# Optimization experiments

Measured on AMD Instinct MI355X. Metric: run time of the kernel, lower is better.

## Reference

```python
import jax, jax.numpy as jnp
import numpy as np

BS, L, D = 16, 256, 512
H, DQ, DV, DFF, KSZ = 8, 64, 64, 2048, 3


def _ln(x, g, b, eps=1e-5):
    mu = jnp.mean(x, -1, keepdims=True)
    var = jnp.mean((x - mu) ** 2, -1, keepdims=True)
    return (x - mu) / jnp.sqrt(var + eps) * g + b


def _conv(x, w):
    # x: [bs, 1, d] (NCW), w: [1, 1, k], same padding for odd k, no bias
    pad = (w.shape[-1] - 1) // 2
    return jax.lax.conv_general_dilated(x, w, (1,), [(pad, pad)], dimension_numbers=('NCH', 'OIH', 'NCH'))


def setup_inputs() -> dict:
    key = jax.random.key(0)
    ks = jax.random.split(key, 12)
    s = lambda k, shape, sc: jax.random.normal(k, shape, jnp.float32) * sc
    w0 = 0.02
    return {
        'inp': jax.random.normal(ks[0], (BS, L, D), jnp.float32),
        'conv1_w': s(ks[1], (1, 1, KSZ), 0.3),
        'conv2_w': s(ks[2], (1, 1, KSZ), 0.3),
        'ctx_wq': s(ks[3], (D, H * DQ), w0),
        'ctx_wk': s(ks[4], (D, H * DQ), w0),
        'ctx_fc': s(ks[5], (H * DV, D), w0),
        'glb_wq': s(ks[6], (D, H * DQ), w0),
        'glb_wk': s(ks[7], (D, H * DQ), w0),
        'glb_fc': s(ks[8], (H * DV, D), w0),
        'ln1_g': jnp.ones(D), 'ln1_b': jnp.zeros(D),
        'ln2_g': jnp.ones(D), 'ln2_b': jnp.zeros(D),
        'ln3_g': jnp.ones(D), 'ln3_b': jnp.zeros(D),
        'mlp_w1': s(ks[9], (D, DFF), w0), 'mlp_b1': jnp.zeros(DFF),
        'mlp_w2': s(ks[10], (DFF, D), w0), 'mlp_b2': jnp.zeros(D),
    }


def reference(inp, conv1_w, conv2_w, ctx_wq, ctx_wk, ctx_fc,
              glb_wq, glb_wk, glb_fc, ln1_g, ln1_b, ln2_g, ln2_b,
              ln3_g, ln3_b, mlp_w1, mlp_b1, mlp_w2, mlp_b2):
    bs, seqlen, d = inp.shape
    scale = 1.0 / jnp.sqrt(jnp.float32(DQ))
    # Global K/V are step-invariant: hoist out of the recurrence.
    # NOTE: original module (faithfully) projects V with W_Q, not W_V.
    Kg = (inp @ glb_wk).reshape(bs, seqlen, H, DQ).transpose(0, 2, 1, 3)  # [b,h,L,dq]
    Vg = (inp @ glb_wq).reshape(bs, seqlen, H, DV).transpose(0, 2, 1, 3)  # [b,h,L,dv]

    def step(hn, x_i):
        # hn: [bs,1,d] recurrent state, x_i: [bs,d] current token
        x = x_i[:, None, :]                                   # [bs,1,d]
        res = x
        xc = _conv(x, conv1_w)                                # [bs,1,d]
        # context cross-attn: Q=hn, K=xc, V=xc (via W_Q, as in source)
        Qc = (hn @ ctx_wq).reshape(bs, 1, H, DQ).transpose(0, 2, 1, 3)
        Kc = (xc @ ctx_wk).reshape(bs, 1, H, DQ).transpose(0, 2, 1, 3)
        Vc = (xc @ ctx_wq).reshape(bs, 1, H, DV).transpose(0, 2, 1, 3)
        sc = jnp.einsum('bhqd,bhkd->bhqk', Qc, Kc) * scale    # [b,h,1,1]
        ac = jax.nn.softmax(sc, axis=-1)
        ctx = jnp.einsum('bhqk,bhkd->bhqd', ac, Vc)
        ctx = ctx.transpose(0, 2, 1, 3).reshape(bs, 1, H * DV) @ ctx_fc
        x = _ln(ctx + res, ln1_g, ln1_b)
        res = x
        x2 = _conv(x, conv2_w)
        # global cross-attn: Q=x2, K/V from full input (hoisted)
        Qg = (x2 @ glb_wq).reshape(bs, 1, H, DQ).transpose(0, 2, 1, 3)
        sg = jnp.einsum('bhqd,bhkd->bhqk', Qg, Kg) * scale    # [b,h,1,L]
        h = jnp.einsum('bhqk,bhkd->bhqd', jax.nn.softmax(sg, axis=-1), Vg)
        h = h.transpose(0, 2, 1, 3).reshape(bs, 1, H * DV) @ glb_fc  # [bs,1,d]
        x = _ln(h + res, ln2_g, ln2_b)
        y = jax.nn.gelu(x @ mlp_w1 + mlp_b1, approximate=False) @ mlp_w2 + mlp_b2
        y = _ln(y + x, ln3_g, ln3_b)
        return h, y[:, 0, :]

    hn0 = inp[:, 0:1, :]
    hn, ys = jax.lax.scan(step, hn0, jnp.swapaxes(inp, 0, 1))  # ys: [L,bs,d]
    output = jnp.swapaxes(ys, 0, 1)                            # [bs,L,d]
    return output, hn
```

## Files before the change

### kernel.cpp

```cpp
#include <hip/hip_runtime.h>
#include <math.h>

#define NBS 16
#define NL 256
#define ND 512
#define NH 8
#define NDFF 2048
#define NT (NBS*NL)

typedef unsigned short u16;
typedef unsigned int   u32;
typedef __attribute__((ext_vector_type(8))) short bf16x8;
typedef __attribute__((ext_vector_type(4))) float f32x4;

__device__ __forceinline__ u16 f2b(float f){
  u32 u = __float_as_uint(f);
  u32 r = u + 0x7FFFu + ((u >> 16) & 1u);
  return (u16)(r >> 16);
}
__device__ __forceinline__ float blo(u32 u){ return __uint_as_float(u << 16); }
__device__ __forceinline__ float bhi(u32 u){ return __uint_as_float(u & 0xFFFF0000u); }
__device__ __forceinline__ float b2f(u16 v){ return __uint_as_float(((u32)v) << 16); }
__device__ __forceinline__ u32 pk2(float a, float b){ return (u32)f2b(a) | ((u32)f2b(b) << 16); }

__device__ __forceinline__ void gl16(const void* g, void* l){
  __builtin_amdgcn_global_load_lds((const __attribute__((address_space(1))) void*)g,
                                   (__attribute__((address_space(3))) void*)l, 16, 0, 0);
}
__device__ __forceinline__ float gelu_f(float x){ return 0.5f*x*(1.f+erff(x*0.70710678118654752f)); }

__device__ inline void tr_tile(const float* __restrict__ src, u16* __restrict__ dst,
                               int K, int N, int ntk, int tb, float* Tsh){
  int tk = tb % ntk, tn = tb / ntk;
  int t = threadIdx.x;
  int r = t >> 2, q = t & 3;
  const float* s = src + (size_t)(tk*64 + r)*N + tn*64 + q*16;
  #pragma unroll
  for (int u2 = 0; u2 < 4; u2++){
    float4 v = *(const float4*)(s + u2*4);
    Tsh[r*65 + q*16 + u2*4 + 0] = v.x;
    Tsh[r*65 + q*16 + u2*4 + 1] = v.y;
    Tsh[r*65 + q*16 + u2*4 + 2] = v.z;
    Tsh[r*65 + q*16 + u2*4 + 3] = v.w;
  }
  __syncthreads();
  int n = t >> 2, kq = t & 3;
  u16* d = dst + (size_t)(tn*64 + n)*K + tk*64 + kq*16;
  u32 u[8];
  #pragma unroll
  for (int j = 0; j < 8; j++){
    u32 lo = f2b(Tsh[(kq*16 + 2*j    )*65 + n]);
    u32 hi = f2b(Tsh[(kq*16 + 2*j + 1)*65 + n]);
    u[j] = lo | (hi << 16);
  }
  ((uint4*)d)[0] = make_uint4(u[0],u[1],u[2],u[3]);
  ((uint4*)d)[1] = make_uint4(u[4],u[5],u[6],u[7]);
}

__global__ __launch_bounds__(256) void pack_k(
    const float* __restrict__ inp,
    const float* __restrict__ ctx_wq, const float* __restrict__ ctx_fc,
    const float* __restrict__ glb_wq, const float* __restrict__ glb_wk,
    const float* __restrict__ glb_fc,
    const float* __restrict__ w1, const float* __restrict__ w2,
    const float* __restrict__ c1w,
    u16* wk_t, u16* wq_t, u16* cfc_t, u16* gfc_t, u16* cwq_bf,
    u16* w1_t, u16* w2_t, u16* inp_bf, u16* xc_bf)
{
  __shared__ float Tsh[64*65];
  int bx = blockIdx.x, t = threadIdx.x;
  if (bx < 256){
    int m = bx >> 6, tb = bx & 63;
    const float* s; u16* d;
    if      (m == 0){ s = glb_wk; d = wk_t; }
    else if (m == 1){ s = glb_wq; d = wq_t; }
    else if (m == 2){ s = ctx_fc; d = cfc_t; }
    else            { s = glb_fc; d = gfc_t; }
    tr_tile(s, d, 512, 512, 8, tb, Tsh);
  } else if (bx < 512){
    tr_tile(w1, w1_t, 512, 2048, 8, bx - 256, Tsh);
  } else if (bx < 768){
    tr_tile(w2, w2_t, 2048, 512, 32, bx - 512, Tsh);
  } else if (bx < 1792){
    size_t i0 = (size_t)(bx - 768)*2048 + (size_t)t*8;
    float4 v0 = *(const float4*)(inp + i0);
    float4 v1 = *(const float4*)(inp + i0 + 4);
    uint4 o;
    o.x = pk2(v0.x, v0.y); o.y = pk2(v0.z, v0.w);
    o.z = pk2(v1.x, v1.y); o.w = pk2(v1.z, v1.w);
    *(uint4*)(inp_bf + i0) = o;
  } else if (bx < 2816){
    size_t i0 = (size_t)(bx - 1792)*2048 + (size_t)t*8;
    float w0 = c1w[0], w1v = c1w[1], w2v = c1w[2];
    u32 u[4];
    #pragma unroll
    for (int j = 0; j < 8; j += 2){
      float f[2];
      #pragma unroll
      for (int s2 = 0; s2 < 2; s2++){
        size_t i = i0 + j + s2; int d = (int)(i & (ND-1));
        float xm = d        ? inp[i-1] : 0.f;
        float x0 = inp[i];
        float xp = (d<ND-1) ? inp[i+1] : 0.f;
        f[s2] = w0*xm + w1v*x0 + w2v*xp;
      }
      u[j>>1] = pk2(f[0], f[1]);
    }
    *(uint4*)(xc_bf + i0) = make_uint4(u[0],u[1],u[2],u[3]);
  } else {
    size_t i0 = (size_t)(bx - 2816)*2048 + (size_t)t*8;
    float4 v0 = *(const float4*)(ctx_wq + i0);
    float4 v1 = *(const float4*)(ctx_wq + i0 + 4);
    uint4 o;
    o.x = pk2(v0.x, v0.y); o.y = pk2(v0.z, v0.w);
    o.z = pk2(v1.x, v1.y); o.w = pk2(v1.z, v1.w);
    *(uint4*)(cwq_bf + i0) = o;
  }
}

template<int TM,int BIAS,int ACT>
__device__ __forceinline__ void gemm_core(const u16* __restrict__ A,
    const u16* __restrict__ Bt, const float* __restrict__ bias,
    void* __restrict__ Cb, int N, int K, int lda, int ldb, int outm,
    u16* sm, int row0, int col0)
{
  constexpr int MF = TM/32;
  constexpr int ABUF = TM*128;
  constexpr int NLD = TM/32 + 2;
  const int tid = threadIdx.x;
  const int w = tid >> 6, l = tid & 63;
  const int wr = w >> 1, wc = w & 1;
  const int srow = tid >> 3;
  const int scol = (((tid & 7)*16) ^ ((srow & 7) << 4)) >> 1;
  const u16* pa = A  + (size_t)(row0 + srow)*lda + scol;
  const u16* pb = Bt + (size_t)(col0 + srow)*ldb + scol;
  char* lA0 = (char*)sm + (tid & ~63)*16;
  char* lB0 = (char*)sm + 3*ABUF + (tid & ~63)*16;

  f32x4 acc[MF][2] = {};
  const int l15 = l & 15, lk = (l >> 4)*16;
  const int nt = K >> 6;

  auto STAGE = [&](int buf, int kt){
    char* lA = lA0 + buf*ABUF;
    char* lB = lB0 + buf*8192;
    #pragma unroll
    for (int i = 0; i < TM/32; i++)
      gl16(pa + kt*64 + (size_t)(i*32)*lda, lA + i*4096);
    gl16(pb + kt*64,                  lB);
    gl16(pb + kt*64 + (size_t)32*ldb, lB + 4096);
  };

  STAGE(0, 0);
  int cur = 0, nxt = 1;
  for (int t = 0; t < nt; ++t){
    if (t + 1 < nt){
      STAGE(nxt, t + 1);
      if constexpr (NLD == 4) asm volatile("s_waitcnt vmcnt(4)" ::: "memory");
      else                    asm volatile("s_waitcnt vmcnt(6)" ::: "memory");
    } else {
      asm volatile("s_waitcnt vmcnt(0)" ::: "memory");
    }
    __builtin_amdgcn_s_barrier();
    __builtin_amdgcn_sched_barrier(0);
    const char* bA = (const char*)sm + cur*ABUF;
    const char* bB = (const char*)sm + 3*ABUF + cur*8192;
    #pragma unroll
    for (int ks = 0; ks < 2; ks++){
      bf16x8 af[MF], bv[2];
      #pragma unroll
      for (int m = 0; m < MF; m++){
        int r = wr*(TM/2) + m*16 + l15;
        int cb = (ks*64 + lk) ^ ((r & 7) << 4);
        af[m] = *(const bf16x8*)(bA + r*128 + cb);
      }
      #pragma unroll
      for (int n = 0; n < 2; n++){
        int r = wc*32 + n*16 + l15;
        int cb = (ks*64 + lk) ^ ((r & 7) << 4);
        bv[n] = *(const bf16x8*)(bB + r*128 + cb);
      }
      #pragma unroll
      for (int m = 0; m < MF; m++)
        #pragma unroll
        for (int n = 0; n < 2; n++)
          acc[m][n] = __builtin_amdgcn_mfma_f32_16x16x32_bf16(af[m], bv[n], acc[m][n], 0, 0, 0);
    }
    cur = nxt; nxt = (nxt == 2) ? 0 : nxt + 1;
  }

  #pragma unroll
  for (int m = 0; m < MF; m++){
    #pragma unroll
    for (int n = 0; n < 2; n++){
      int col = col0 + wc*32 + n*16 + l15;
      int rowb = row0 + wr*(TM/2) + m*16 + (l >> 4)*4;
      if (outm == 2){
        uint2 o;
        o.x = pk2(acc[m][n][0], acc[m][n][1]);
        o.y = pk2(acc[m][n][2], acc[m][n][3]);
        *(uint2*)((u16*)Cb + (size_t)(rowb >> 8)*131072 + (size_t)col*256 + (rowb & 255)) = o;
      } else if (outm == 0){
        #pragma unroll
        for (int rr = 0; rr < 4; rr++)
          ((float*)Cb)[(size_t)(rowb + rr)*N + col] = acc[m][n][rr];
      } else {
        #pragma unroll
        for (int rr = 0; rr < 4; rr++){
          float v = acc[m][n][rr];
          if (BIAS) v += bias[col];
          if (ACT)  v = gelu_f(v);
          ((u16*)Cb)[(size_t)(rowb + rr)*N + col] = f2b(v);
        }
      }
    }
  }
}

template<int TM,int BIAS,int ACT,int OUTM>
__global__ __launch_bounds__(256) void gemm_k(const u16* __restrict__ A,
                                              const u16* __restrict__ Bt,
                                              const float* __restrict__ bias,
                                              void* __restrict__ Cb,
                                              int N, int K)
{
  __shared__ u16 sm[3*(TM*128 + 8192)/2];
  gemm_core<TM,BIAS,ACT>(A, Bt, bias, Cb, N, K, K, K, OUTM, sm,
                         blockIdx.y*TM, blockIdx.x*64);
}

__global__ __launch_bounds__(256) void gemm3_k(
    const u16* __restrict__ A0, const u16* __restrict__ B0, u16* __restrict__ C0,
    const u16* __restrict__ A1, const u16* __restrict__ B1, u16* __restrict__ C1,
    const u16* __restrict__ A2, const u16* __restrict__ B2, u16* __restrict__ C2)
{
  __shared__ u16 sm[3*(64*128 + 8192)/2];
  const u16 *A, *Bt; u16* Cb; int outm = 1;
  if (blockIdx.z == 0){ A = A0; Bt = B0; Cb = C0; }
  else if (blockIdx.z == 1){ A = A1; Bt = B1; Cb = C1; outm = 2; }
  else { A = A2; Bt = B2; Cb = C2; }
  gemm_core<64,0,0>(A, Bt, nullptr, Cb, 512, 512, 512, 512, outm, sm,
                    blockIdx.y*64, blockIdx.x*64);
}

__global__ __launch_bounds__(256) void gemm_w2sk(const u16* __restrict__ G,
                                                 const u16* __restrict__ w2t,
                                                 float* __restrict__ P)
{
  __shared__ u16 sm[3*(128*128 + 8192)/2];
  const int z = blockIdx.z;
  gemm_core<128,0,0>(G + z*1024, w2t + z*1024, nullptr,
                     (void*)(P + (size_t)z*NT*512), 512, 1024, 2048, 2048, 0,
                     sm, blockIdx.y*128, blockIdx.x*64);
}

__global__ __launch_bounds__(256) void attn_k(const u16* __restrict__ Q,
                                              const u16* __restrict__ Kg,
                                              const u16* __restrict__ Vt,
                                              u16* __restrict__ O){
  __shared__ u16 sm[36864];
  const int bh = blockIdx.x, b = bh >> 3, h = bh & 7;
  const int tid = threadIdx.x;
  const int w = tid >> 6, l = tid & 63;
  const int l15 = l & 15, lg = l >> 4;
  const int qt0 = b*NL + blockIdx.y*64 + w*16;

  {
    const int srow = tid >> 3;
    const int scolK = (((tid & 7)*16) ^ ((srow & 7) << 4)) >> 1;
    const u16* pk = Kg + (size_t)(b*NL + srow)*ND + h*64 + scolK;
    char* lK = (char*)sm + (tid & ~63)*16;
    #pragma unroll
    for (int c = 0; c < 8; c++)
      gl16(pk + (size_t)(c*32)*ND, lK + c*4096);
  }
  {
    const int vrow = tid >> 5;
    const int vcb = (tid*16) & 511;
    const int scolV = (vcb ^ ((vrow & 7) << 4)) >> 1;
    const u16* pv = Vt + (size_t)bh*16384 + (size_t)vrow*256 + scolV;
    char* lV = (char*)sm + 32768 + (tid & ~63)*16;
    #pragma unroll
    for (int c = 0; c < 8; c++)
      gl16(pv + (size_t)(c*8)*256, lV + c*4096);
  }

  bf16x8 aq[2];
  {
    const u16* qp = Q + (size_t)(qt0 + l15)*ND + h*64 + lg*8;
    aq[0] = *(const bf16x8*)(qp);
    aq[1] = *(const bf16x8*)(qp + 32);
  }
  char* Pw = (char*)sm + 65536 + w*2048;

  f32x4 oacc[4] = {};
  float rsum[4] = {0.f, 0.f, 0.f, 0.f};
  __syncthreads();

  #pragma unroll
  for (int c = 0; c < 4; c++){
    f32x4 sacc[4] = {};
    #pragma unroll
    for (int n = 0; n < 4; n++){
      int r = c*64 + n*16 + l15;
      #pragma unroll
      for (int ks = 0; ks < 2; ks++){
        int cb = r*128 + ((ks*64 + lg*16) ^ ((r & 7) << 4));
        bf16x8 bk = *(const bf16x8*)((const char*)sm + cb);
        sacc[n] = __builtin_amdgcn_mfma_f32_16x16x32_bf16(aq[ks], bk, sacc[n], 0, 0, 0);
      }
    }
    #pragma unroll
    for (int n = 0; n < 4; n++){
      #pragma unroll
      for (int rr = 0; rr < 4; rr++){
        float p = __expf(sacc[n][rr]*0.125f);
        rsum[rr] += p;
        int q = lg*4 + rr, key = n*16 + l15;
        int byte = (q*128 + key*2) ^ ((q & 7) << 4);
        *(u16*)(Pw + byte) = f2b(p);
      }
    }
    bf16x8 ap[2];
    #pragma unroll
    for (int ks2 = 0; ks2 < 2; ks2++){
      int cb = (ks2*64 + lg*16) ^ ((l15 & 7) << 4);
      ap[ks2] = *(const bf16x8*)(Pw + l15*128 + cb);
    }
    #pragma unroll
    for (int n = 0; n < 4; n++){
      int r = n*16 + l15;
      #pragma unroll
      for (int ks2 = 0; ks2 < 2; ks2++){
        int cb = 32768 + r*512 + ((c*128 + ks2*64 + lg*16) ^ ((r & 7) << 4));
        bf16x8 bvv = *(const bf16x8*)((const char*)sm + cb);
        oacc[n] = __builtin_amdgcn_mfma_f32_16x16x32_bf16(ap[ks2], bvv, oacc[n], 0, 0, 0);
      }
    }
  }

  #pragma unroll
  for (int m = 1; m < 16; m <<= 1){
    #pragma unroll
    for (int rr = 0; rr < 4; rr++) rsum[rr] += __shfl_xor(rsum[rr], m);
  }
  float inv[4];
  #pragma unroll
  for (int rr = 0; rr < 4; rr++) inv[rr] = 1.f / rsum[rr];

  #pragma unroll
  for (int n = 0; n < 4; n++){
    int d = h*64 + n*16 + l15;
    #pragma unroll
    for (int rr = 0; rr < 4; rr++){
      int t = qt0 + lg*4 + rr;
      O[(size_t)t*ND + d] = f2b(oacc[n][rr]*inv[rr]);
    }
  }
}

template<int MODE>
__global__ __launch_bounds__(256) void ln_k(const void* __restrict__ aptr,
                                            const void* __restrict__ bptr,
                                            const float* __restrict__ g,
                                            const float* __restrict__ be,
                                            const float* __restrict__ cw,
                                            const float* __restrict__ a2,
                                            const float* __restrict__ bias2,
                                            u16* __restrict__ obf,
                                            u16* __restrict__ convbf,
                                            float* __restrict__ of32,
                                            float* __restrict__ hnout)
{
  __shared__ float row[512];
  __shared__ float red[10];
  const int r0 = blockIdx.x, tid = threadIdx.x;
  const size_t base = (size_t)r0*ND;
  const int d = tid*2;
  float v0, v1;
  if (MODE == 3){
    float2 p0 = *(const float2*)((const float*)aptr + base + d);
    float2 p1 = *(const float2*)(a2 + base + d);
    u32 bv = *(const u32*)((const u16*)bptr + base + d);
    v0 = p0.x + p1.x + bias2[d]   + blo(bv);
    v1 = p0.y + p1.y + bias2[d+1] + bhi(bv);
  } else {
    u32 av = *(const u32*)((const u16*)aptr + base + d);
    v0 = blo(av); v1 = bhi(av);
    if (MODE == 1 && (r0 & 255) == 255){
      hnout[(size_t)(r0 >> 8)*512 + d]     = v0;
      hnout[(size_t)(r0 >> 8)*512 + d + 1] = v1;
    }
    if (MODE == 0){
      float2 bv = *(const float2*)((const float*)bptr + base + d);
      v0 += bv.x; v1 += bv.y;
    } else {
      u32 bv = *(const u32*)((const u16*)bptr + base + d);
      v0 += blo(bv); v1 += bhi(bv);
    }
  }
  float s = v0+v1, ss = v0*v0+v1*v1;
  #pragma unroll
  for (int m = 1; m < 64; m <<= 1){ s += __shfl_xor(s, m); ss += __shfl_xor(ss, m); }
  int wv = tid >> 6;
  if ((tid & 63) == 0){ red[wv] = s; red[4+wv] = ss; }
  __syncthreads();
  if (tid == 0){
    float S = red[0]+red[1]+red[2]+red[3];
    float SS = red[4]+red[5]+red[6]+red[7];
    float mu = S*(1.f/ND);
    float var = SS*(1.f/ND) - mu*mu;
    red[8] = mu; red[9] = rsqrtf(var + 1e-5f);
  }
  __syncthreads();
  float mu = red[8], rsd = red[9];
  float o0 = (v0-mu)*rsd*g[d]   + be[d];
  float o1 = (v1-mu)*rsd*g[d+1] + be[d+1];
  if (MODE == 3){
    *(float2*)(of32 + base + d) = make_float2(o0, o1);
  } else {
    *(u32*)(obf + base + d) = pk2(o0, o1);
    if (MODE == 0){
      row[d] = o0; row[d+1] = o1;
      __syncthreads();
      float w0 = cw[0], w1v = cw[1], w2v = cw[2];
      float xm = d ? row[d-1] : 0.f;
      float xp2 = (d+2 < 512) ? row[d+2] : 0.f;
      float c0 = w0*xm + w1v*o0 + w2v*o1;
      float c1 = w0*o0 + w1v*o1 + w2v*xp2;
      *(u32*)(convbf + base + d) = pk2(c0, c1);
    }
  }
}

extern "C" void kernel_launch(void* const* d_in, const int* in_sizes, int n_in,
                              void* d_out, int out_size, void* d_ws, size_t ws_size,
                              hipStream_t stream) {
  const float* inp     = (const float*)d_in[0];
  const float* conv1_w = (const float*)d_in[1];
  const float* conv2_w = (const float*)d_in[2];
  const float* ctx_wq  = (const float*)d_in[3];
  const float* ctx_fc  = (const float*)d_in[5];
  const float* glb_wq  = (const float*)d_in[6];
  const float* glb_wk  = (const float*)d_in[7];
  const float* glb_fc  = (const float*)d_in[8];
  const float* ln1_g = (const float*)d_in[9],  *ln1_b = (const float*)d_in[10];
  const float* ln2_g = (const float*)d_in[11], *ln2_b = (const float*)d_in[12];
  const float* ln3_g = (const float*)d_in[13], *ln3_b = (const float*)d_in[14];
  const float* mlp_w1 = (const float*)d_in[15], *mlp_b1 = (const float*)d_in[16];
  const float* mlp_w2 = (const float*)d_in[17], *mlp_b2 = (const float*)d_in[18];
  float* out = (float*)d_out;
  float* hn  = out + (size_t)NT*ND;

  u16* wk_t   = (u16*)d_ws;
  u16* wq_t   = wk_t   + 262144;
  u16* cfc_t  = wq_t   + 262144;
  u16* gfc_t  = cfc_t  + 262144;
  u16* cwq_bf = gfc_t  + 262144;
  u16* Wc_t   = cwq_bf + 262144;
  u16* w1_t   = Wc_t   + 262144;
  u16* w2_t   = w1_t   + 1048576;
  u16* inp_bf = w2_t   + 1048576;
  u16* Abf    = inp_bf + 2097152;
  u16* Bbf    = Abf    + 2097152;
  u16* Cbf    = Bbf    + 2097152;
  u16* Kg     = Cbf    + 2097152;
  u16* Vt     = Kg     + 2097152;
  u16* X1bf   = Vt     + 2097152;
  u16* X3bf   = X1bf   + 2097152;
  u16* Gbf    = X3bf   + 2097152;
  float* Pf   = (float*)(Gbf + 8388608);

  pack_k<<<2944, 256, 0, stream>>>(inp, ctx_wq, ctx_fc, glb_wq, glb_wk, glb_fc,
                                   mlp_w1, mlp_w2, conv1_w,
                                   wk_t, wq_t, cfc_t, gfc_t, cwq_bf, w1_t, w2_t,
                                   inp_bf, Abf);
  gemm_k<64,0,0,1><<<dim3(8,8),256,0,stream>>>(cfc_t, cwq_bf, nullptr, Wc_t, 512, 512);
  gemm3_k<<<dim3(8,64,3),256,0,stream>>>(inp_bf, wk_t, Kg,
                                         inp_bf, wq_t, Vt,
                                         Abf,    Wc_t, Cbf);
  ln_k<0><<<NT,256,0,stream>>>(Cbf, inp, ln1_g, ln1_b, conv2_w, nullptr, nullptr,
                               X1bf, Abf, nullptr, nullptr);
  gemm_k<64,0,0,1><<<dim3(8,64),256,0,stream>>>(Abf, wq_t, nullptr, Bbf, 512, 512);
  attn_k<<<dim3(NBS*NH, 4),256,0,stream>>>(Bbf, Kg, Vt, Abf);
  gemm_k<64,0,0,1><<<dim3(8,64),256,0,stream>>>(Abf, gfc_t, nullptr, Cbf, 512, 512);
  ln_k<1><<<NT,256,0,stream>>>(Cbf, X1bf, ln2_g, ln2_b, nullptr, nullptr, nullptr,
                               X3bf, nullptr, nullptr, hn);
  gemm_k<128,1,1,1><<<dim3(32,32),256,0,stream>>>(X3bf, w1_t, mlp_b1, Gbf, 2048, 512);
  gemm_w2sk<<<dim3(8,32,2),256,0,stream>>>(Gbf, w2_t, Pf);
  ln_k<3><<<NT,256,0,stream>>>(Pf, X3bf, ln3_g, ln3_b, nullptr, Pf + (size_t)NT*512,
                               mlp_b2, nullptr, nullptr, out, nullptr);
}
```

Before: 119.2 us.

## Fuse Q projection into attention kernel and switch GEMMs to 128x128 double-buffered tiles

Merges the global-query projection GEMM into the attention kernel, so each block computes its 64x64 Q tile in LDS before the softmax-attention loop. This removes one launch and one global round trip for Q. The large GEMMs move from 128x64 or 64x64 tiles with a triple-buffered vmcnt pipeline to 128x128 tiles with simple double buffering and __syncthreads. The bigger tiles cut operand reloads but halve the block count and may expose more load latency, and the fused kernel recomputes the Q projection per head block.

```diff
diff --git a/kernel.cpp b/kernel.cpp
--- a/kernel.cpp
+++ b/kernel.cpp
@@ -20,7 +20,6 @@
 }
 __device__ __forceinline__ float blo(u32 u){ return __uint_as_float(u << 16); }
 __device__ __forceinline__ float bhi(u32 u){ return __uint_as_float(u & 0xFFFF0000u); }
-__device__ __forceinline__ float b2f(u16 v){ return __uint_as_float(((u32)v) << 16); }
 __device__ __forceinline__ u32 pk2(float a, float b){ return (u32)f2b(a) | ((u32)f2b(b) << 16); }
 
 __device__ __forceinline__ void gl16(const void* g, void* l){
@@ -118,83 +117,70 @@
   }
 }
 
-template<int TM,int BIAS,int ACT>
-__device__ __forceinline__ void gemm_core(const u16* __restrict__ A,
+template<int BIAS,int ACT>
+__device__ __forceinline__ void gemm128_core(const u16* __restrict__ A,
     const u16* __restrict__ Bt, const float* __restrict__ bias,
     void* __restrict__ Cb, int N, int K, int lda, int ldb, int outm,
     u16* sm, int row0, int col0)
 {
-  constexpr int MF = TM/32;
-  constexpr int ABUF = TM*128;
-  constexpr int NLD = TM/32 + 2;
   const int tid = threadIdx.x;
   const int w = tid >> 6, l = tid & 63;
   const int wr = w >> 1, wc = w & 1;
+  const int l15 = l & 15, lk = (l >> 4)*16;
   const int srow = tid >> 3;
   const int scol = (((tid & 7)*16) ^ ((srow & 7) << 4)) >> 1;
   const u16* pa = A  + (size_t)(row0 + srow)*lda + scol;
   const u16* pb = Bt + (size_t)(col0 + srow)*ldb + scol;
-  char* lA0 = (char*)sm + (tid & ~63)*16;
-  char* lB0 = (char*)sm + 3*ABUF + (tid & ~63)*16;
-
-  f32x4 acc[MF][2] = {};
-  const int l15 = l & 15, lk = (l >> 4)*16;
+  char* lA = (char*)sm + (tid & ~63)*16;
+  char* lB = (char*)sm + 32768 + (tid & ~63)*16;
+
+  f32x4 acc[4][4] = {};
   const int nt = K >> 6;
 
   auto STAGE = [&](int buf, int kt){
-    char* lA = lA0 + buf*ABUF;
-    char* lB = lB0 + buf*8192;
-    #pragma unroll
-    for (int i = 0; i < TM/32; i++)
-      gl16(pa + kt*64 + (size_t)(i*32)*lda, lA + i*4096);
-    gl16(pb + kt*64,                  lB);
-    gl16(pb + kt*64 + (size_t)32*ldb, lB + 4096);
+    char* a = lA + buf*16384;
+    char* b = lB + buf*16384;
+    #pragma unroll
+    for (int i = 0; i < 4; i++){
+      gl16(pa + kt + (size_t)(i*32)*lda, a + i*4096);
+      gl16(pb + kt + (size_t)(i*32)*ldb, b + i*4096);
+    }
   };
 
   STAGE(0, 0);
-  int cur = 0, nxt = 1;
+  __syncthreads();
   for (int t = 0; t < nt; ++t){
-    if (t + 1 < nt){
-      STAGE(nxt, t + 1);
-      if constexpr (NLD == 4) asm volatile("s_waitcnt vmcnt(4)" ::: "memory");
-      else                    asm volatile("s_waitcnt vmcnt(6)" ::: "memory");
-    } else {
-      asm volatile("s_waitcnt vmcnt(0)" ::: "memory");
-    }
-    __builtin_amdgcn_s_barrier();
-    __builtin_amdgcn_sched_barrier(0);
-    const char* bA = (const char*)sm + cur*ABUF;
-    const char* bB = (const char*)sm + 3*ABUF + cur*8192;
+    if (t + 1 < nt) STAGE((t+1) & 1, (t+1)*64);
+    const char* bA = (const char*)sm + (t&1)*16384;
+    const char* bB = (const char*)sm + 32768 + (t&1)*16384;
     #pragma unroll
     for (int ks = 0; ks < 2; ks++){
-      bf16x8 af[MF], bv[2];
-      #pragma unroll
-      for (int m = 0; m < MF; m++){
-        int r = wr*(TM/2) + m*16 + l15;
-        int cb = (ks*64 + lk) ^ ((r & 7) << 4);
-        af[m] = *(const bf16x8*)(bA + r*128 + cb);
-      }
-      #pragma unroll
-      for (int n = 0; n < 2; n++){
-        int r = wc*32 + n*16 + l15;
-        int cb = (ks*64 + lk) ^ ((r & 7) << 4);
-        bv[n] = *(const bf16x8*)(bB + r*128 + cb);
-      }
-      #pragma unroll
-      for (int m = 0; m < MF; m++)
+      bf16x8 af[4], bv[4];
+      #pragma unroll
+      for (int m = 0; m < 4; m++){
+        int r = wr*64 + m*16 + l15;
+        af[m] = *(const bf16x8*)(bA + r*128 + ((ks*64 + lk) ^ ((r & 7) << 4)));
+      }
+      #pragma unroll
+      for (int n = 0; n < 4; n++){
+        int r = wc*64 + n*16 + l15;
+        bv[n] = *(const bf16x8*)(bB + r*128 + ((ks*64 + lk) ^ ((r & 7) << 4)));
+      }
+      #pragma unroll
+      for (int m = 0; m < 4; m++)
         #pragma unroll
-        for (int n = 0; n < 2; n++)
+        for (int n = 0; n < 4; n++)
           acc[m][n] = __builtin_amdgcn_mfma_f32_16x16x32_bf16(af[m], bv[n], acc[m][n], 0, 0, 0);
     }
-    cur = nxt; nxt = (nxt == 2) ? 0 : nxt + 1;
-  }
-
-  #pragma unroll
-  for (int m = 0; m < MF; m++){
-    #pragma unroll
-    for (int n = 0; n < 2; n++){
-      int col = col0 + wc*32 + n*16 + l15;
-      int rowb = row0 + wr*(TM/2) + m*16 + (l >> 4)*4;
+    __syncthreads();
+  }
+
+  #pragma unroll
+  for (int m = 0; m < 4; m++){
+    #pragma unroll
+    for (int n = 0; n < 4; n++){
+      int col = col0 + wc*64 + n*16 + l15;
+      int rowb = row0 + wr*64 + m*16 + (l >> 4)*4;
       if (outm == 2){
         uint2 o;
         o.x = pk2(acc[m][n][0], acc[m][n][1]);
@@ -217,16 +203,15 @@
   }
 }
 
-template<int TM,int BIAS,int ACT,int OUTM>
-__global__ __launch_bounds__(256) void gemm_k(const u16* __restrict__ A,
-                                              const u16* __restrict__ Bt,
-                                              const float* __restrict__ bias,
-                                              void* __restrict__ Cb,
-                                              int N, int K)
-{
-  __shared__ u16 sm[3*(TM*128 + 8192)/2];
-  gemm_core<TM,BIAS,ACT>(A, Bt, bias, Cb, N, K, K, K, OUTM, sm,
-                         blockIdx.y*TM, blockIdx.x*64);
+template<int BIAS,int ACT>
+__global__ __launch_bounds__(256) void gemm128_k(const u16* __restrict__ A,
+                                                 const u16* __restrict__ Bt,
+                                                 const float* __restrict__ bias,
+                                                 void* __restrict__ Cb, int N, int K)
+{
+  __shared__ u16 sm[32768];
+  gemm128_core<BIAS,ACT>(A, Bt, bias, Cb, N, K, K, K, 1, sm,
+                         blockIdx.y*128, blockIdx.x*128);
 }
 
 __global__ __launch_bounds__(256) void gemm3_k(
@@ -234,68 +219,192 @@
     const u16* __restrict__ A1, const u16* __restrict__ B1, u16* __restrict__ C1,
     const u16* __restrict__ A2, const u16* __restrict__ B2, u16* __restrict__ C2)
 {
-  __shared__ u16 sm[3*(64*128 + 8192)/2];
+  __shared__ u16 sm[32768];
   const u16 *A, *Bt; u16* Cb; int outm = 1;
   if (blockIdx.z == 0){ A = A0; Bt = B0; Cb = C0; }
   else if (blockIdx.z == 1){ A = A1; Bt = B1; Cb = C1; outm = 2; }
   else { A = A2; Bt = B2; Cb = C2; }
-  gemm_core<64,0,0>(A, Bt, nullptr, Cb, 512, 512, 512, 512, outm, sm,
-                    blockIdx.y*64, blockIdx.x*64);
+  gemm128_core<0,0>(A, Bt, nullptr, Cb, 512, 512, 512, 512, outm, sm,
+                    blockIdx.y*128, blockIdx.x*128);
 }
 
 __global__ __launch_bounds__(256) void gemm_w2sk(const u16* __restrict__ G,
                                                  const u16* __restrict__ w2t,
                                                  float* __restrict__ P)
 {
-  __shared__ u16 sm[3*(128*128 + 8192)/2];
+  __shared__ u16 sm[32768];
   const int z = blockIdx.z;
-  gemm_core<128,0,0>(G + z*1024, w2t + z*1024, nullptr,
-                     (void*)(P + (size_t)z*NT*512), 512, 1024, 2048, 2048, 0,
-                     sm, blockIdx.y*128, blockIdx.x*64);
-}
-
-__global__ __launch_bounds__(256) void attn_k(const u16* __restrict__ Q,
-                                              const u16* __restrict__ Kg,
-                                              const u16* __restrict__ Vt,
-                                              u16* __restrict__ O){
-  __shared__ u16 sm[36864];
-  const int bh = blockIdx.x, b = bh >> 3, h = bh & 7;
+  gemm128_core<0,0>(G + z*1024, w2t + z*1024, nullptr,
+                    (void*)(P + (size_t)z*NT*512), 512, 1024, 2048, 2048, 0,
+                    sm, blockIdx.y*128, blockIdx.x*128);
+}
+
+__global__ __launch_bounds__(256) void gemm64_k(const u16* __restrict__ A,
+                                                const u16* __restrict__ Bt,
+                                                u16* __restrict__ Cb, int N, int K)
+{
+  __shared__ u16 sm[16384];
+  const int tid = threadIdx.x;
+  const int w = tid >> 6, l = tid & 63;
+  const int wr = w >> 1, wc = w & 1;
+  const int l15 = l & 15, lk = (l >> 4)*16;
+  const int row0 = blockIdx.y*64, col0 = blockIdx.x*64;
+  const int srow = tid >> 3;
+  const int scol = (((tid & 7)*16) ^ ((srow & 7) << 4)) >> 1;
+  const u16* pa = A  + (size_t)(row0 + srow)*K + scol;
+  const u16* pb = Bt + (size_t)(col0 + srow)*K + scol;
+  char* lA = (char*)sm + (tid & ~63)*16;
+
+  f32x4 acc[2][2] = {};
+  const int nt = K >> 6;
+  auto STAGE = [&](int buf, int kt){
+    char* a = lA + buf*8192;
+    char* b = lA + 16384 + buf*8192;
+    gl16(pa + kt,                a);
+    gl16(pa + kt + (size_t)32*K, a + 4096);
+    gl16(pb + kt,                b);
+    gl16(pb + kt + (size_t)32*K, b + 4096);
+  };
+  STAGE(0, 0);
+  __syncthreads();
+  for (int t = 0; t < nt; ++t){
+    if (t + 1 < nt) STAGE((t+1) & 1, (t+1)*64);
+    const char* bA = (const char*)sm + (t&1)*8192;
+    const char* bB = (const char*)sm + 16384 + (t&1)*8192;
+    #pragma unroll
+    for (int ks = 0; ks < 2; ks++){
+      bf16x8 af[2], bv[2];
+      #pragma unroll
+      for (int m = 0; m < 2; m++){
+        int r = wr*32 + m*16 + l15;
+        af[m] = *(const bf16x8*)(bA + r*128 + ((ks*64 + lk) ^ ((r & 7) << 4)));
+      }
+      #pragma unroll
+      for (int n = 0; n < 2; n++){
+        int r = wc*32 + n*16 + l15;
+        bv[n] = *(const bf16x8*)(bB + r*128 + ((ks*64 + lk) ^ ((r & 7) << 4)));
+      }
+      #pragma unroll
+      for (int m = 0; m < 2; m++)
+        #pragma unroll
+        for (int n = 0; n < 2; n++)
+          acc[m][n] = __builtin_amdgcn_mfma_f32_16x16x32_bf16(af[m], bv[n], acc[m][n], 0, 0, 0);
+    }
+    __syncthreads();
+  }
+  #pragma unroll
+  for (int m = 0; m < 2; m++){
+    #pragma unroll
+    for (int n = 0; n < 2; n++){
+      int col = col0 + wc*32 + n*16 + l15;
+      int rowb = row0 + wr*32 + m*16 + (l >> 4)*4;
+      #pragma unroll
+      for (int rr = 0; rr < 4; rr++)
+        Cb[(size_t)(rowb + rr)*N + col] = f2b(acc[m][n][rr]);
+    }
+  }
+}
+
+__global__ __launch_bounds__(256) void qattn_k(const u16* __restrict__ X2,
+                                               const u16* __restrict__ Wq,
+                                               const u16* __restrict__ Kg,
+                                               const u16* __restrict__ Vt,
+                                               u16* __restrict__ O)
+{
+  __shared__ u16 sm[40960];
+  const int h = blockIdx.x, ty = blockIdx.y;
+  const int b = ty >> 2, bh = b*8 + h;
   const int tid = threadIdx.x;
   const int w = tid >> 6, l = tid & 63;
   const int l15 = l & 15, lg = l >> 4;
-  const int qt0 = b*NL + blockIdx.y*64 + w*16;
-
-  {
-    const int srow = tid >> 3;
-    const int scolK = (((tid & 7)*16) ^ ((srow & 7) << 4)) >> 1;
-    const u16* pk = Kg + (size_t)(b*NL + srow)*ND + h*64 + scolK;
-    char* lK = (char*)sm + (tid & ~63)*16;
-    #pragma unroll
-    for (int c = 0; c < 8; c++)
-      gl16(pk + (size_t)(c*32)*ND, lK + c*4096);
-  }
+  const int wr = w >> 1, wc = w & 1;
+  const int lk = lg*16;
+
   {
     const int vrow = tid >> 5;
-    const int vcb = (tid*16) & 511;
+    const int vcb  = (tid*16) & 511;
     const int scolV = (vcb ^ ((vrow & 7) << 4)) >> 1;
     const u16* pv = Vt + (size_t)bh*16384 + (size_t)vrow*256 + scolV;
-    char* lV = (char*)sm + 32768 + (tid & ~63)*16;
+    char* lV = (char*)sm + 40960 + (tid & ~63)*16;
     #pragma unroll
     for (int c = 0; c < 8; c++)
       gl16(pv + (size_t)(c*8)*256, lV + c*4096);
   }
 
+  const int srow = tid >> 3;
+  const int scol = (((tid & 7)*16) ^ ((srow & 7) << 4)) >> 1;
+  const u16* pa = X2 + (size_t)(ty*64 + srow)*512 + scol;
+  const u16* pb = Wq + (size_t)(h*64  + srow)*512 + scol;
+  char* lS = (char*)sm + (tid & ~63)*16;
+
+  auto QSTG = [&](int buf, int kt){
+    char* a = lS + buf*8192;
+    char* bq = lS + 16384 + buf*8192;
+    gl16(pa + kt,              a);
+    gl16(pa + kt + 32*512,     a + 4096);
+    gl16(pb + kt,              bq);
+    gl16(pb + kt + 32*512,     bq + 4096);
+  };
+
+  f32x4 qacc[2][2] = {};
+  QSTG(0, 0);
+  __syncthreads();
+  for (int t = 0; t < 8; ++t){
+    if (t < 7) QSTG((t+1) & 1, (t+1)*64);
+    const char* bA = (const char*)sm + (t&1)*8192;
+    const char* bB = (const char*)sm + 16384 + (t&1)*8192;
+    #pragma unroll
+    for (int ks = 0; ks < 2; ks++){
+      bf16x8 af[2], bv[2];
+      #pragma unroll
+      for (int m = 0; m < 2; m++){
+        int r = wr*32 + m*16 + l15;
+        af[m] = *(const bf16x8*)(bA + r*128 + ((ks*64 + lk) ^ ((r & 7) << 4)));
+      }
+      #pragma unroll
+      for (int n = 0; n < 2; n++){
+        int r = wc*32 + n*16 + l15;
+        bv[n] = *(const bf16x8*)(bB + r*128 + ((ks*64 + lk) ^ ((r & 7) << 4)));
+      }
+      #pragma unroll
+      for (int m = 0; m < 2; m++)
+        #pragma unroll
+        for (int n = 0; n < 2; n++)
+          qacc[m][n] = __builtin_amdgcn_mfma_f32_16x16x32_bf16(af[m], bv[n], qacc[m][n], 0, 0, 0);
+    }
+    __syncthreads();
+  }
+
+  {
+    const u16* pk = Kg + (size_t)(b*256 + srow)*512 + h*64 + scol;
+    char* lK = (char*)sm + (tid & ~63)*16;
+    #pragma unroll
+    for (int c = 0; c < 8; c++)
+      gl16(pk + (size_t)(c*32)*512, lK + c*4096);
+  }
+  #pragma unroll
+  for (int m = 0; m < 2; m++)
+    #pragma unroll
+    for (int n = 0; n < 2; n++)
+      #pragma unroll
+      for (int rr = 0; rr < 4; rr++){
+        int row = wr*32 + m*16 + (l >> 4)*4 + rr;
+        int col = wc*32 + n*16 + l15;
+        *(u16*)((char*)sm + 32768 + row*128 + ((col*2) ^ ((row & 7) << 4))) = f2b(qacc[m][n][rr]);
+      }
+  __syncthreads();
+
+  const int qt0 = b*256 + (ty & 3)*64 + w*16;
   bf16x8 aq[2];
-  {
-    const u16* qp = Q + (size_t)(qt0 + l15)*ND + h*64 + lg*8;
-    aq[0] = *(const bf16x8*)(qp);
-    aq[1] = *(const bf16x8*)(qp + 32);
-  }
-  char* Pw = (char*)sm + 65536 + w*2048;
+  #pragma unroll
+  for (int ks = 0; ks < 2; ks++){
+    int qr = w*16 + l15;
+    aq[ks] = *(const bf16x8*)((char*)sm + 32768 + qr*128 + ((ks*64 + lk) ^ ((qr & 7) << 4)));
+  }
+  char* Pw = (char*)sm + 73728 + w*2048;
 
   f32x4 oacc[4] = {};
   float rsum[4] = {0.f, 0.f, 0.f, 0.f};
-  __syncthreads();
 
   #pragma unroll
   for (int c = 0; c < 4; c++){
@@ -305,8 +414,7 @@
       int r = c*64 + n*16 + l15;
       #pragma unroll
       for (int ks = 0; ks < 2; ks++){
-        int cb = r*128 + ((ks*64 + lg*16) ^ ((r & 7) << 4));
-        bf16x8 bk = *(const bf16x8*)((const char*)sm + cb);
+        bf16x8 bk = *(const bf16x8*)((const char*)sm + r*128 + ((ks*64 + lk) ^ ((r & 7) << 4)));
         sacc[n] = __builtin_amdgcn_mfma_f32_16x16x32_bf16(aq[ks], bk, sacc[n], 0, 0, 0);
       }
     }
@@ -317,23 +425,20 @@
         float p = __expf(sacc[n][rr]*0.125f);
         rsum[rr] += p;
         int q = lg*4 + rr, key = n*16 + l15;
-        int byte = (q*128 + key*2) ^ ((q & 7) << 4);
-        *(u16*)(Pw + byte) = f2b(p);
+        *(u16*)(Pw + ((q*128 + key*2) ^ ((q & 7) << 4))) = f2b(p);
       }
     }
     bf16x8 ap[2];
     #pragma unroll
-    for (int ks2 = 0; ks2 < 2; ks2++){
-      int cb = (ks2*64 + lg*16) ^ ((l15 & 7) << 4);
-      ap[ks2] = *(const bf16x8*)(Pw + l15*128 + cb);
-    }
+    for (int ks2 = 0; ks2 < 2; ks2++)
+      ap[ks2] = *(const bf16x8*)(Pw + l15*128 + ((ks2*64 + lk) ^ ((l15 & 7) << 4)));
     #pragma unroll
     for (int n = 0; n < 4; n++){
       int r = n*16 + l15;
       #pragma unroll
       for (int ks2 = 0; ks2 < 2; ks2++){
-        int cb = 32768 + r*512 + ((c*128 + ks2*64 + lg*16) ^ ((r & 7) << 4));
-        bf16x8 bvv = *(const bf16x8*)((const char*)sm + cb);
+        bf16x8 bvv = *(const bf16x8*)((const char*)sm + 40960 + r*512 +
+                                      ((c*128 + ks2*64 + lk) ^ ((r & 7) << 4)));
         oacc[n] = __builtin_amdgcn_mfma_f32_16x16x32_bf16(ap[ks2], bvv, oacc[n], 0, 0, 0);
       }
     }
@@ -344,17 +449,13 @@
     #pragma unroll
     for (int rr = 0; rr < 4; rr++) rsum[rr] += __shfl_xor(rsum[rr], m);
   }
-  float inv[4];
-  #pragma unroll
-  for (int rr = 0; rr < 4; rr++) inv[rr] = 1.f / rsum[rr];
-
   #pragma unroll
   for (int n = 0; n < 4; n++){
     int d = h*64 + n*16 + l15;
     #pragma unroll
     for (int rr = 0; rr < 4; rr++){
       int t = qt0 + lg*4 + rr;
-      O[(size_t)t*ND + d] = f2b(oacc[n][rr]*inv[rr]);
+      O[(size_t)t*ND + d] = f2b(oacc[n][rr]/rsum[rr]);
     }
   }
 }
@@ -475,19 +576,18 @@
                                    mlp_w1, mlp_w2, conv1_w,
                                    wk_t, wq_t, cfc_t, gfc_t, cwq_bf, w1_t, w2_t,
                                    inp_bf, Abf);
-  gemm_k<64,0,0,1><<<dim3(8,8),256,0,stream>>>(cfc_t, cwq_bf, nullptr, Wc_t, 512, 512);
-  gemm3_k<<<dim3(8,64,3),256,0,stream>>>(inp_bf, wk_t, Kg,
+  gemm64_k<<<dim3(8,8),256,0,stream>>>(cfc_t, cwq_bf, Wc_t, 512, 512);
+  gemm3_k<<<dim3(4,32,3),256,0,stream>>>(inp_bf, wk_t, Kg,
                                          inp_bf, wq_t, Vt,
                                          Abf,    Wc_t, Cbf);
   ln_k<0><<<NT,256,0,stream>>>(Cbf, inp, ln1_g, ln1_b, conv2_w, nullptr, nullptr,
                                X1bf, Abf, nullptr, nullptr);
-  gemm_k<64,0,0,1><<<dim3(8,64),256,0,stream>>>(Abf, wq_t, nullptr, Bbf, 512, 512);
-  attn_k<<<dim3(NBS*NH, 4),256,0,stream>>>(Bbf, Kg, Vt, Abf);
-  gemm_k<64,0,0,1><<<dim3(8,64),256,0,stream>>>(Abf, gfc_t, nullptr, Cbf, 512, 512);
+  qattn_k<<<dim3(8,64),256,0,stream>>>(Abf, wq_t, Kg, Vt, Bbf);
+  gemm64_k<<<dim3(8,64),256,0,stream>>>(Bbf, gfc_t, Cbf, 512, 512);
   ln_k<1><<<NT,256,0,stream>>>(Cbf, X1bf, ln2_g, ln2_b, nullptr, nullptr, nullptr,
                                X3bf, nullptr, nullptr, hn);
-  gemm_k<128,1,1,1><<<dim3(32,32),256,0,stream>>>(X3bf, w1_t, mlp_b1, Gbf, 2048, 512);
-  gemm_w2sk<<<dim3(8,32,2),256,0,stream>>>(Gbf, w2_t, Pf);
+  gemm128_k<1,1><<<dim3(16,32),256,0,stream>>>(X3bf, w1_t, mlp_b1, Gbf, 2048, 512);
+  gemm_w2sk<<<dim3(4,32,2),256,0,stream>>>(Gbf, w2_t, Pf);
   ln_k<3><<<NT,256,0,stream>>>(Pf, X3bf, ln3_g, ln3_b, nullptr, Pf + (size_t)NT*512,
                                mlp_b2, nullptr, nullptr, out, nullptr);
 }
```

After: 104.3 us. 12.5% less time.
